# Optimization experiments

Hardware: AMD Instinct MI355X
Metric: run time of the kernel (lower is better)

The kernel has to match this reference:

```python
import jax, jax.numpy as jnp
import numpy as np

D_MODEL = 1024
N_HEADS = 16
D_HEAD = 64
D_FF = 4096
BATCH = 4
SEQ = 2048
EPS = 1e-05


def gelu_lean(x):
    cubic = x * x * x
    cdf = 0.5 * (1.0 + jnp.tanh(0.7978845608 * (x + 0.044715 * cubic)))
    return x * cdf


def layernorm(x, gamma, beta):
    mean = jnp.mean(x, axis=-1, keepdims=True)
    var = jnp.mean((x - mean) ** 2, axis=-1, keepdims=True)
    return gamma * ((x - mean) / jnp.sqrt(var + EPS)) + beta


def setup_inputs() -> dict:
    key = jax.random.key(0)
    ks = jax.random.split(key, 8)
    std = 0.02
    return {
        "x": jax.random.normal(ks[0], (BATCH, SEQ, D_MODEL), dtype=jnp.float32),
        "gamma1": jnp.ones((D_MODEL,), jnp.float32),
        "beta1": jnp.zeros((D_MODEL,), jnp.float32),
        "wq": std * jax.random.normal(ks[1], (N_HEADS, D_HEAD, D_MODEL), dtype=jnp.float32),
        "wk": std * jax.random.normal(ks[2], (N_HEADS, D_HEAD, D_MODEL), dtype=jnp.float32),
        "wv": std * jax.random.normal(ks[3], (N_HEADS, D_HEAD, D_MODEL), dtype=jnp.float32),
        "wo": std * jax.random.normal(ks[4], (D_MODEL, N_HEADS * D_HEAD), dtype=jnp.float32),
        "gamma2": jnp.ones((D_MODEL,), jnp.float32),
        "beta2": jnp.zeros((D_MODEL,), jnp.float32),
        "mlp_fc1": std * jax.random.normal(ks[5], (D_FF, D_MODEL), dtype=jnp.float32),
        "mlp_fc2": std * jax.random.normal(ks[6], (D_MODEL, D_FF), dtype=jnp.float32),
    }


def reference(x, gamma1, beta1, wq, wk, wv, wo, gamma2, beta2, mlp_fc1, mlp_fc2):
    n = layernorm(x, gamma1, beta1)  # [B,S,D]
    scale = jnp.sqrt(jnp.float32(D_HEAD))
    # per-head projections, vectorized over heads: [B,S,H,dh]
    q = jnp.einsum("bsd,hed->bshe", n, wq)
    k = jnp.einsum("bsd,hed->bshe", n, wk)
    v = jnp.einsum("bsd,hed->bshe", n, wv)
    scores = jnp.einsum("bqhe,bkhe->bhqk", q, k) / scale  # [B,H,S,S]
    seq = x.shape[1]
    mask = jnp.triu(jnp.ones((seq, seq), dtype=bool), k=1)
    scores = jnp.where(mask, jnp.float32(-1e9), scores)
    weights = jax.nn.softmax(scores, axis=-1)
    attn = jnp.einsum("bhqk,bkhe->bqhe", weights, v)  # [B,S,H,dh]
    concat = attn.reshape(x.shape[0], seq, N_HEADS * D_HEAD)  # head-order concat
    attn_out = concat @ wo.T
    x_resid = x + attn_out
    n2 = layernorm(x_resid, gamma2, beta2)
    hidden = gelu_lean(n2 @ mlp_fc1.T)
    mlp_out = hidden @ mlp_fc2.T
    return x_resid + mlp_out
```

## Files before the change

### kernel.cpp

```cpp
#include <hip/hip_runtime.h>
#include <hip/hip_bf16.h>

#define D_MODEL 1024
#define N_HEADS 16
#define D_HEAD  64
#define D_FF    4096
#define BATCH   4
#define SEQ     2048
#define ROWS    (BATCH*SEQ)
#define LN_EPS  1e-5f

typedef __bf16 bf16;
typedef __bf16 bf16x8 __attribute__((ext_vector_type(8)));
typedef float  f32x4  __attribute__((ext_vector_type(4)));

__device__ __forceinline__ void load16_lds(const bf16* g, bf16* l) {
#if defined(__has_builtin) && __has_builtin(__builtin_amdgcn_global_load_lds)
    __builtin_amdgcn_global_load_lds(
        (const __attribute__((address_space(1))) unsigned int*)g,
        (__attribute__((address_space(3))) unsigned int*)l,
        16, 0, 0);
#else
    const int lane = threadIdx.x & 63;
    ((bf16x8*)l)[lane] = *(const bf16x8*)g;
#endif
}

__global__ __launch_bounds__(256) void f2b4_kernel(const float* a, const float* b,
                                                   const float* c, const float* d,
                                                   bf16* oa, bf16* ob, bf16* oc, bf16* od,
                                                   int n) {
    const float* srcs[4] = {a, b, c, d};
    bf16* dsts[4] = {oa, ob, oc, od};
    const float* s = srcs[blockIdx.y];
    bf16* dst = dsts[blockIdx.y];
    int i = blockIdx.x * 256 + threadIdx.x;
    int stride = gridDim.x * 256;
    for (; i < n; i += stride) dst[i] = (bf16)s[i];
}
__global__ __launch_bounds__(256) void f2b2_kernel(const float* a, const float* b,
                                                   bf16* oa, bf16* ob, int n) {
    const float* s = blockIdx.y ? b : a;
    bf16* dst = blockIdx.y ? ob : oa;
    int i = blockIdx.x * 256 + threadIdx.x;
    int stride = gridDim.x * 256;
    for (; i < n; i += stride) dst[i] = (bf16)s[i];
}

__global__ __launch_bounds__(256) void ln_kernel(const float* __restrict__ x,
                                                 const float* __restrict__ gamma,
                                                 const float* __restrict__ beta,
                                                 bf16* __restrict__ out) {
    const int row = blockIdx.x;
    const int tid = threadIdx.x;
    const float* xr = x + (size_t)row * D_MODEL;

    float vals[4];
    float s = 0.f, ss = 0.f;
#pragma unroll
    for (int t = 0; t < 4; ++t) {
        float v = xr[tid + t * 256];
        vals[t] = v;
        s += v;
        ss += v * v;
    }
#pragma unroll
    for (int off = 32; off > 0; off >>= 1) {
        s  += __shfl_xor(s, off, 64);
        ss += __shfl_xor(ss, off, 64);
    }
    __shared__ float sbuf[4], ssbuf[4];
    const int wave = tid >> 6;
    if ((tid & 63) == 0) { sbuf[wave] = s; ssbuf[wave] = ss; }
    __syncthreads();
    s  = sbuf[0] + sbuf[1] + sbuf[2] + sbuf[3];
    ss = ssbuf[0] + ssbuf[1] + ssbuf[2] + ssbuf[3];

    const float mean = s * (1.f / D_MODEL);
    const float var  = ss * (1.f / D_MODEL) - mean * mean;
    const float inv  = rsqrtf(var + LN_EPS);

    bf16* orow = out + (size_t)row * D_MODEL;
#pragma unroll
    for (int t = 0; t < 4; ++t) {
        int c = tid + t * 256;
        orow[c] = (bf16)(gamma[c] * ((vals[t] - mean) * inv) + beta[c]);
    }
}

__device__ __forceinline__ float gelu_f(float x) {
    float c = x * x * x;
    return 0.5f * x * (1.f + tanhf(0.7978845608f * (x + 0.044715f * c)));
}

template <int EPI, int TN, typename OutT>
__global__ __launch_bounds__(256) void gemm_mt(const bf16* __restrict__ A,
                                               const bf16* __restrict__ W,
                                               OutT* C,
                                               const float* ADD,
                                               bf16* VT,
                                               int M, int N, int K) {
    constexpr int WN = TN / 64;
    constexpr int WM = 4 / WN;
    constexpr int SM = (128 / WM) / 16;

    __shared__ __align__(16) bf16 sA[128 * 32];
    __shared__ __align__(16) bf16 sB[TN * 32];
    __shared__ __align__(16) bf16 tbuf[EPI == 4 ? 4 * 64 * 72 : 4];

    const int wave = threadIdx.x >> 6;
    const int lane = threadIdx.x & 63;
    const int quad = lane >> 4;
    const int l16  = lane & 15;
    const int wm   = wave / WN;
    const int wn   = wave % WN;

    const int nN  = N / TN;
    const int b   = blockIdx.x;
    const int xcd = b & 7;
    const int j   = b >> 3;
    const int bx  = j % nN;
    const int band = (j / nN) * 8 + xcd;

    const int m0 = band * 128;
    const int n0 = bx * TN;

    const int srow = lane >> 2;
    const int scol = (lane & 3) * 8;
    const bf16* gA0 = A + (size_t)(m0 + wave * 32 + srow) * K + scol;
    const bf16* gA1 = gA0 + (size_t)16 * K;
    bf16* lA0 = &sA[(wave * 32) * 32];
    bf16* lA1 = &sA[(wave * 32 + 16) * 32];
    const bf16* gB0 = W + (size_t)(n0 + wave * (TN / 4) + srow) * K + scol;
    const bf16* gB1 = gB0 + (size_t)16 * K;
    bf16* lB0 = &sB[(wave * (TN / 4)) * 32];
    bf16* lB1 = &sB[(wave * (TN / 4) + 16) * 32];

    f32x4 acc[SM][4] = {};

    for (int k0 = 0; k0 < K; k0 += 32) {
        load16_lds(gA0 + k0, lA0);
        load16_lds(gA1 + k0, lA1);
        load16_lds(gB0 + k0, lB0);
        if constexpr (TN == 128) load16_lds(gB1 + k0, lB1);
        __syncthreads();

        bf16x8 af[SM], bfr[4];
#pragma unroll
        for (int s = 0; s < SM; ++s)
            af[s] = *reinterpret_cast<const bf16x8*>(&sA[(wm * (128 / WM) + s * 16 + l16) * 32 + quad * 8]);
#pragma unroll
        for (int t = 0; t < 4; ++t)
            bfr[t] = *reinterpret_cast<const bf16x8*>(&sB[(wn * 64 + t * 16 + l16) * 32 + quad * 8]);
#pragma unroll
        for (int s = 0; s < SM; ++s)
#pragma unroll
            for (int t = 0; t < 4; ++t)
                acc[s][t] = __builtin_amdgcn_mfma_f32_16x16x32_bf16(af[s], bfr[t], acc[s][t], 0, 0, 0);
        __syncthreads();
    }

    if constexpr (EPI == 4) {
        if (n0 >= 2048) {
            bf16* tw = &tbuf[wave * 64 * 72];
#pragma unroll
            for (int s = 0; s < SM; ++s)
#pragma unroll
                for (int t = 0; t < 4; ++t)
#pragma unroll
                    for (int r = 0; r < 4; ++r)
                        tw[(t * 16 + l16) * 72 + s * 16 + quad * 4 + r] = (bf16)acc[s][t][r];
#pragma unroll
            for (int i = 0; i < 8; ++i) {
                const int flat = i * 64 + lane;
                const int nl = flat >> 3;
                const int mc = flat & 7;
                bf16x8 v = *reinterpret_cast<const bf16x8*>(&tw[nl * 72 + mc * 8]);
                const int vcol = n0 - 2048 + wn * 64 + nl;
                const int m_glob = m0 + wm * 64 + mc * 8;
                const int bb = m_glob >> 11, sp = m_glob & (SEQ - 1);
                const int hh = vcol >> 6,  dh = vcol & 63;
                const size_t tidx = (((size_t)(bb * N_HEADS + hh) * D_HEAD + dh) << 11) + sp;
                *reinterpret_cast<bf16x8*>(&VT[tidx]) = v;
            }
        } else {
            const float qscale = (n0 < 1024) ? 0.125f : 1.0f;
#pragma unroll
            for (int s = 0; s < SM; ++s) {
                const int mbase = m0 + wm * (128 / WM) + s * 16 + quad * 4;
#pragma unroll
                for (int t = 0; t < 4; ++t) {
                    const int n = n0 + wn * 64 + t * 16 + l16;
#pragma unroll
                    for (int r = 0; r < 4; ++r)
                        C[(size_t)(mbase + r) * 2048 + n] = (OutT)(acc[s][t][r] * qscale);
                }
            }
        }
    } else {
#pragma unroll
        for (int s = 0; s < SM; ++s) {
            const int mbase = m0 + wm * (128 / WM) + s * 16 + quad * 4;
#pragma unroll
            for (int t = 0; t < 4; ++t) {
                const int n = n0 + wn * 64 + t * 16 + l16;
#pragma unroll
                for (int r = 0; r < 4; ++r) {
                    float v = acc[s][t][r];
                    if (EPI == 1) v = gelu_f(v);
                    const size_t idx = (size_t)(mbase + r) * N + n;
                    if (EPI == 2) v += ADD[idx];
                    C[idx] = (OutT)v;
                }
            }
        }
    }
}

__global__ __launch_bounds__(256) void flash_attn_kernel(const bf16* __restrict__ qk,
                                                         const bf16* __restrict__ vt,
                                                         bf16* __restrict__ o) {
    const int id   = blockIdx.x;
    const int bhl  = id & 7;
    const int rest = id >> 3;
    const int pair = rest & 15;
    const int bhh  = rest >> 4;
    const int bh   = bhh * 8 + bhl;
    const int b    = bh >> 4;
    const int h    = bh & 15;
    const int wave = threadIdx.x >> 6;
    const int lane = threadIdx.x & 63;
    const int quad = lane >> 4;
    const int l16  = lane & 15;

    __shared__ __align__(16) bf16 sK[64 * 64];
    __shared__ __align__(16) bf16 sV[64 * 64];
    __shared__ bf16 pbuf[4][16][68];

    const bf16* kbase = qk + (size_t)(b * SEQ) * 2048 + 1024 + h * D_HEAD;
    const bf16* vbase = vt + ((size_t)(bh * D_HEAD) << 11);

    const int lrow   = lane >> 3;
    const int lchunk = (lane & 7) ^ lrow;
    const int xr     = l16 & 7;

    bf16x8 ones;
#pragma unroll
    for (int i = 0; i < 8; ++i) ones[i] = (bf16)1.0f;

    for (int half = 0; half < 2; ++half) {
        const int qtile = half ? 31 - pair : pair;
        const int q0 = qtile * 64 + wave * 16;
        const size_t qrow = (size_t)(b * SEQ + q0 + l16) * 2048 + h * D_HEAD;
        bf16x8 qf0 = *reinterpret_cast<const bf16x8*>(qk + qrow + quad * 8);
        bf16x8 qf1 = *reinterpret_cast<const bf16x8*>(qk + qrow + 32 + quad * 8);

        f32x4 o_acc[4] = {(f32x4)(0.f), (f32x4)(0.f), (f32x4)(0.f), (f32x4)(0.f)};
        float m_q = -1e30f;
        float l_r[4] = {0.f, 0.f, 0.f, 0.f};

        for (int jt = 0; jt <= qtile; ++jt) {
            const int j0 = jt * 64;
            const bf16* gk = kbase + (size_t)(j0 + wave * 16 + lrow) * 2048 + lchunk * 8;
            const bf16* gv = vbase + (size_t)(wave * 16 + lrow) * 2048 + j0 + lchunk * 8;
            load16_lds(gk,            &sK[(wave * 16) * 64]);
            load16_lds(gk + 8 * 2048, &sK[(wave * 16 + 8) * 64]);
            load16_lds(gv,            &sV[(wave * 16) * 64]);
            load16_lds(gv + 8 * 2048, &sV[(wave * 16 + 8) * 64]);
            __syncthreads();

            f32x4 s_acc[4] = {(f32x4)(0.f), (f32x4)(0.f), (f32x4)(0.f), (f32x4)(0.f)};
#pragma unroll
            for (int nb = 0; nb < 4; ++nb) {
                const int row = nb * 16 + l16;
                const int slot = quad ^ xr;
                bf16x8 kf0 = *reinterpret_cast<const bf16x8*>(&sK[row * 64 + slot * 8]);
                bf16x8 kf1 = *reinterpret_cast<const bf16x8*>(&sK[row * 64 + (slot ^ 4) * 8]);
                s_acc[nb] = __builtin_amdgcn_mfma_f32_16x16x32_bf16(qf0, kf0, s_acc[nb], 0, 0, 0);
                s_acc[nb] = __builtin_amdgcn_mfma_f32_16x16x32_bf16(qf1, kf1, s_acc[nb], 0, 0, 0);
            }
            const bool diag = (jt == qtile);
            float sv[4][4];
            float mx = -1e30f;
#pragma unroll
            for (int nb = 0; nb < 4; ++nb) {
                const int key = j0 + nb * 16 + l16;
#pragma unroll
                for (int r = 0; r < 4; ++r) {
                    float s = s_acc[nb][r];
                    if (diag && key > q0 + quad * 4 + r) s = -1e30f;
                    sv[nb][r] = s;
                    mx = fmaxf(mx, s);
                }
            }
#pragma unroll
            for (int off = 1; off < 16; off <<= 1) mx = fmaxf(mx, __shfl_xor(mx, off, 64));
            const float mn = fmaxf(m_q, mx);
            const float alpha = __expf(m_q - mn);
            m_q = mn;
#pragma unroll
            for (int nb = 0; nb < 4; ++nb)
#pragma unroll
                for (int r = 0; r < 4; ++r)
                    pbuf[wave][quad * 4 + r][nb * 16 + l16] = (bf16)__expf(sv[nb][r] - mn);
#pragma unroll
            for (int r = 0; r < 4; ++r) l_r[r] *= alpha;
#pragma unroll
            for (int nb = 0; nb < 4; ++nb) o_acc[nb] *= alpha;
            bf16x8 pf0 = *reinterpret_cast<const bf16x8*>(&pbuf[wave][l16][quad * 8]);
            bf16x8 pf1 = *reinterpret_cast<const bf16x8*>(&pbuf[wave][l16][32 + quad * 8]);
            f32x4 lt = (f32x4)(0.f);
            lt = __builtin_amdgcn_mfma_f32_16x16x32_bf16(pf0, ones, lt, 0, 0, 0);
            lt = __builtin_amdgcn_mfma_f32_16x16x32_bf16(pf1, ones, lt, 0, 0, 0);
#pragma unroll
            for (int r = 0; r < 4; ++r) l_r[r] += lt[r];
#pragma unroll
            for (int nb = 0; nb < 4; ++nb) {
                const int row = nb * 16 + l16;
                const int slot = quad ^ xr;
                bf16x8 vf0 = *reinterpret_cast<const bf16x8*>(&sV[row * 64 + slot * 8]);
                bf16x8 vf1 = *reinterpret_cast<const bf16x8*>(&sV[row * 64 + (slot ^ 4) * 8]);
                o_acc[nb] = __builtin_amdgcn_mfma_f32_16x16x32_bf16(pf0, vf0, o_acc[nb], 0, 0, 0);
                o_acc[nb] = __builtin_amdgcn_mfma_f32_16x16x32_bf16(pf1, vf1, o_acc[nb], 0, 0, 0);
            }
            __syncthreads();
        }
#pragma unroll
        for (int nb = 0; nb < 4; ++nb) {
#pragma unroll
            for (int r = 0; r < 4; ++r) {
                const int qrow_g = q0 + quad * 4 + r;
                o[(size_t)(b * SEQ + qrow_g) * D_MODEL + h * D_HEAD + nb * 16 + l16] =
                    (bf16)(o_acc[nb][r] / l_r[r]);
            }
        }
    }
}

extern "C" void kernel_launch(void* const* d_in, const int* in_sizes, int n_in,
                              void* d_out, int out_size, void* d_ws, size_t ws_size,
                              hipStream_t stream) {
    const float* x      = (const float*)d_in[0];
    const float* gamma1 = (const float*)d_in[1];
    const float* beta1  = (const float*)d_in[2];
    const float* wq     = (const float*)d_in[3];
    const float* wk     = (const float*)d_in[4];
    const float* wv     = (const float*)d_in[5];
    const float* wo     = (const float*)d_in[6];
    const float* gamma2 = (const float*)d_in[7];
    const float* beta2  = (const float*)d_in[8];
    const float* fc1    = (const float*)d_in[9];
    const float* fc2    = (const float*)d_in[10];
    float* out = (float*)d_out;

    const size_t WSMALL = (size_t)N_HEADS * D_HEAD * D_MODEL;
    const size_t WFF    = (size_t)D_FF * D_MODEL;
    const size_t RD     = (size_t)ROWS * D_MODEL;

    char* wsb = (char*)d_ws;
    bf16* wq_b  = (bf16*)(wsb);
    bf16* wk_b  = wq_b + WSMALL;
    bf16* wv_b  = wk_b + WSMALL;
    bf16* wo_b  = wv_b + WSMALL;
    bf16* fc1_b = wo_b + WSMALL;
    bf16* fc2_b = fc1_b + WFF;
    bf16* slotA = fc2_b + WFF;
    bf16* qkb   = slotA + RD;
    bf16* vtb   = qkb + 2 * RD;

    bf16* n1    = slotA;
    bf16* attnb = slotA;
    bf16* hid   = slotA;
    float* resid = out;

    const size_t need_single = (size_t)(24 + 64 + 16) * 1024 * 1024;
    const bool single = ws_size >= need_single;
    bf16* n2 = single ? (bf16*)(wsb + (size_t)88 * 1024 * 1024) : vtb;

    f2b4_kernel<<<dim3(64, 4), 256, 0, stream>>>(wq, wk, wv, wo, wq_b, wk_b, wv_b, wo_b, (int)WSMALL);
    f2b2_kernel<<<dim3(256, 2), 256, 0, stream>>>(fc1, fc2, fc1_b, fc2_b, (int)WFF);

    ln_kernel<<<ROWS, 256, 0, stream>>>(x, gamma1, beta1, n1);
    gemm_mt<4, 128, bf16><<<(3072 / 128) * (ROWS / 128), 256, 0, stream>>>(n1, wq_b, qkb, nullptr, vtb, ROWS, 3072, D_MODEL);
    flash_attn_kernel<<<1024, 256, 0, stream>>>(qkb, vtb, attnb);
    gemm_mt<2, 64, float><<<(D_MODEL / 64) * (ROWS / 128), 256, 0, stream>>>(attnb, wo_b, resid, x, nullptr, ROWS, D_MODEL, D_MODEL);
    ln_kernel<<<ROWS, 256, 0, stream>>>(resid, gamma2, beta2, n2);

    if (single) {
        gemm_mt<1, 128, bf16><<<(D_FF / 128) * (ROWS / 128), 256, 0, stream>>>(n2, fc1_b, hid, nullptr, nullptr, ROWS, D_FF, D_MODEL);
        gemm_mt<2, 64, float><<<(D_MODEL / 64) * (ROWS / 128), 256, 0, stream>>>(hid, fc2_b, out, resid, nullptr, ROWS, D_MODEL, D_FF);
    } else {
        const int CHUNK = 4096;
        for (int c = 0; c < ROWS / CHUNK; ++c) {
            const bf16*  n2c    = n2    + (size_t)c * CHUNK * D_MODEL;
            const float* residc = resid + (size_t)c * CHUNK * D_MODEL;
            float*       outc   = out   + (size_t)c * CHUNK * D_MODEL;
            gemm_mt<1, 128, bf16><<<(D_FF / 128) * (CHUNK / 128), 256, 0, stream>>>(n2c, fc1_b, hid, nullptr, nullptr, CHUNK, D_FF, D_MODEL);
            gemm_mt<2, 64, float><<<(D_MODEL / 64) * (CHUNK / 128), 256, 0, stream>>>(hid, fc2_b, outc, residc, nullptr, CHUNK, D_MODEL, D_FF);
        }
    }
}
```

Before: 587.0 us.

## Double-buffer K/V tiles in flash attention and use exp-based GELU

The attention loop now keeps two LDS buffers for K and V and issues the async global-to-LDS loads for the next key tile before computing on the current one, so load latency can overlap with the MFMA and softmax work. The GELU epilogue swaps tanhf for an algebraically equivalent sigmoid form built on __expf, which is cheaper on the ALU. LDS use for K/V doubles, which may lower occupancy. The single remaining barrier at the end of each iteration has to cover both the read-after-write on the prefetched buffer and the reuse of the buffer being overwritten.

New measurement: 586.5 us. Within noise of the previous version (-0.1%).

```diff
diff --git a/kernel.cpp b/kernel.cpp
--- a/kernel.cpp
+++ b/kernel.cpp
@@ -89,8 +89,8 @@
 }
 
 __device__ __forceinline__ float gelu_f(float x) {
-    float c = x * x * x;
-    return 0.5f * x * (1.f + tanhf(0.7978845608f * (x + 0.044715f * c)));
+    const float y = x * (0.7978845608f + 0.0356774081f * x * x);
+    return x / (1.f + __expf(-2.f * y));
 }
 
 template <int EPI, int TN, typename OutT>
@@ -233,8 +233,8 @@
     const int quad = lane >> 4;
     const int l16  = lane & 15;
 
-    __shared__ __align__(16) bf16 sK[64 * 64];
-    __shared__ __align__(16) bf16 sV[64 * 64];
+    __shared__ __align__(16) bf16 sK[2][64 * 64];
+    __shared__ __align__(16) bf16 sV[2][64 * 64];
     __shared__ bf16 pbuf[4][16][68];
 
     const bf16* kbase = qk + (size_t)(b * SEQ) * 2048 + 1024 + h * D_HEAD;
@@ -243,6 +243,15 @@
     const int lrow   = lane >> 3;
     const int lchunk = (lane & 7) ^ lrow;
     const int xr     = l16 & 7;
+
+    auto stage = [&](int j0, int buf) {
+        const bf16* gk = kbase + (size_t)(j0 + wave * 16 + lrow) * 2048 + lchunk * 8;
+        const bf16* gv = vbase + (size_t)(wave * 16 + lrow) * 2048 + j0 + lchunk * 8;
+        load16_lds(gk,            &sK[buf][(wave * 16) * 64]);
+        load16_lds(gk + 8 * 2048, &sK[buf][(wave * 16 + 8) * 64]);
+        load16_lds(gv,            &sV[buf][(wave * 16) * 64]);
+        load16_lds(gv + 8 * 2048, &sV[buf][(wave * 16 + 8) * 64]);
+    };
 
     bf16x8 ones;
 #pragma unroll
@@ -259,23 +268,24 @@
         float m_q = -1e30f;
         float l_r[4] = {0.f, 0.f, 0.f, 0.f};
 
+        stage(0, 0);
+        __syncthreads();
+
         for (int jt = 0; jt <= qtile; ++jt) {
             const int j0 = jt * 64;
-            const bf16* gk = kbase + (size_t)(j0 + wave * 16 + lrow) * 2048 + lchunk * 8;
-            const bf16* gv = vbase + (size_t)(wave * 16 + lrow) * 2048 + j0 + lchunk * 8;
-            load16_lds(gk,            &sK[(wave * 16) * 64]);
-            load16_lds(gk + 8 * 2048, &sK[(wave * 16 + 8) * 64]);
-            load16_lds(gv,            &sV[(wave * 16) * 64]);
-            load16_lds(gv + 8 * 2048, &sV[(wave * 16 + 8) * 64]);
-            __syncthreads();
+            const int cur = jt & 1;
+            if (jt < qtile) stage(j0 + 64, cur ^ 1);
+
+            const bf16* sKc = sK[cur];
+            const bf16* sVc = sV[cur];
 
             f32x4 s_acc[4] = {(f32x4)(0.f), (f32x4)(0.f), (f32x4)(0.f), (f32x4)(0.f)};
 #pragma unroll
             for (int nb = 0; nb < 4; ++nb) {
                 const int row = nb * 16 + l16;
                 const int slot = quad ^ xr;
-                bf16x8 kf0 = *reinterpret_cast<const bf16x8*>(&sK[row * 64 + slot * 8]);
-                bf16x8 kf1 = *reinterpret_cast<const bf16x8*>(&sK[row * 64 + (slot ^ 4) * 8]);
+                bf16x8 kf0 = *reinterpret_cast<const bf16x8*>(&sKc[row * 64 + slot * 8]);
+                bf16x8 kf1 = *reinterpret_cast<const bf16x8*>(&sKc[row * 64 + (slot ^ 4) * 8]);
                 s_acc[nb] = __builtin_amdgcn_mfma_f32_16x16x32_bf16(qf0, kf0, s_acc[nb], 0, 0, 0);
                 s_acc[nb] = __builtin_amdgcn_mfma_f32_16x16x32_bf16(qf1, kf1, s_acc[nb], 0, 0, 0);
             }
@@ -318,8 +328,8 @@
             for (int nb = 0; nb < 4; ++nb) {
                 const int row = nb * 16 + l16;
                 const int slot = quad ^ xr;
-                bf16x8 vf0 = *reinterpret_cast<const bf16x8*>(&sV[row * 64 + slot * 8]);
-                bf16x8 vf1 = *reinterpret_cast<const bf16x8*>(&sV[row * 64 + (slot ^ 4) * 8]);
+                bf16x8 vf0 = *reinterpret_cast<const bf16x8*>(&sVc[row * 64 + slot * 8]);
+                bf16x8 vf1 = *reinterpret_cast<const bf16x8*>(&sVc[row * 64 + (slot ^ 4) * 8]);
                 o_acc[nb] = __builtin_amdgcn_mfma_f32_16x16x32_bf16(pf0, vf0, o_acc[nb], 0, 0, 0);
                 o_acc[nb] = __builtin_amdgcn_mfma_f32_16x16x32_bf16(pf1, vf1, o_acc[nb], 0, 0, 0);
             }
```
